# Performance work log

Measured on AMD Instinct MI355X. Metric: run time of the kernel, lower is better.

## Reference

```python
import jax, jax.numpy as jnp
import numpy as np

T, N, F, H = 64, 8192, 256, 256
LN_EPS = 1e-5


def setup_inputs() -> dict:
    key = jax.random.key(0)
    ks = jax.random.split(key, 8)
    bound = 1.0 / np.sqrt(H)  # torch RNNCell init: U(-1/sqrt(H), 1/sqrt(H))
    u = lambda k, shape: jax.random.uniform(k, shape, jnp.float32, -bound, bound)
    return {
        "X": jax.random.normal(ks[0], (T, N, F), jnp.float32),
        "W_ih": u(ks[1], (H, F)),
        "W_hh": u(ks[2], (H, H)),
        "b_ih": u(ks[3], (H,)),
        "b_hh": u(ks[4], (H,)),
        "ln_w": jnp.ones((H,), jnp.float32),
        "ln_b": jnp.zeros((H,), jnp.float32),
    }


def reference(X, W_ih, W_hh, b_ih, b_hh, ln_w, ln_b):
    # Precompute input projections for all steps: [T, N, H]
    Xw = jnp.einsum('tnf,hf->tnh', X, W_ih) + b_ih
    # init == 0 branch: h = X[0] @ W_ih^T + b_hh + b_ih  (no relu)
    h0 = Xw[0] + b_hh

    def step(h, xw_t):
        # RNNCell relu: relu(x W_ih^T + b_ih + h W_hh^T + b_hh)
        h_new = jax.nn.relu(xw_t + h @ W_hh.T + b_hh)
        return h_new, h_new

    _, outs = jax.lax.scan(step, h0, Xw)  # outs: [T, N, H]

    # LayerNorm over last dim
    mean = jnp.mean(outs, axis=-1, keepdims=True)
    var = jnp.var(outs, axis=-1, keepdims=True)
    outs = (outs - mean) * jax.lax.rsqrt(var + LN_EPS) * ln_w + ln_b
    # dropout: identity in eval mode
    return outs
```

## Files before the change

### kernel.cpp

```cpp
#include <hip/hip_runtime.h>
#include <hip/hip_bf16.h>

#define TSTEPS 64
#define NTOT   8192
#define FDIM   256
#define HDIM   256
#define ROWS   32
#define NTHR   256

typedef __attribute__((ext_vector_type(8))) short bf16x8;
typedef __attribute__((ext_vector_type(4))) float f32x4;

__device__ __forceinline__ short f2bf(float f) {
    union { float f; unsigned u; } v; v.f = f;
    unsigned r = v.u + 0x7FFFu + ((v.u >> 16) & 1u);
    return (short)(r >> 16);
}

__global__ __launch_bounds__(NTHR, 1)
void rnn_ln_fused(const float* __restrict__ X,
                  const float* __restrict__ W_ih,
                  const float* __restrict__ W_hh,
                  const float* __restrict__ b_ih,
                  const float* __restrict__ b_hh,
                  const float* __restrict__ ln_w,
                  const float* __restrict__ ln_b,
                  float* __restrict__ out)
{
    extern __shared__ char smem[];
    char*  xbuf = smem;
    char*  hbuf = smem + 16384;
    float* psum = (float*)(smem + 32768);
    float* mrs  = (float*)(smem + 32768 + 1024);

    const int tid = threadIdx.x;
    const int lane = tid & 63;
    const int wv  = tid >> 6;
    const int l15 = lane & 15;
    const int l4  = lane >> 4;
    const int n0  = blockIdx.x * ROWS;

    bf16x8 wih[8][4], whh[8][4];
    #pragma unroll
    for (int kk = 0; kk < 8; ++kk) {
        #pragma unroll
        for (int tc = 0; tc < 4; ++tc) {
            const int wr = wv*64 + tc*16 + l15;
            const int wk = kk*32 + l4*8;
            const float* p = W_ih + wr*FDIM + wk;
            const float* q = W_hh + wr*HDIM + wk;
            bf16x8 fi, fh;
            #pragma unroll
            for (int e = 0; e < 8; ++e) { fi[e] = f2bf(p[e]); fh[e] = f2bf(q[e]); }
            wih[kk][tc] = fi; whh[kk][tc] = fh;
        }
    }

    float bc[4], lw[4], lb[4];
    #pragma unroll
    for (int tc = 0; tc < 4; ++tc) {
        const int c = wv*64 + tc*16 + l15;
        bc[tc] = b_ih[c] + b_hh[c];
        lw[tc] = ln_w[c];
        lb[tc] = ln_b[c];
    }

    f32x4 acc[2][4];
    f32x4 xld[8];

    auto load_x = [&](int t) {
        const f32x4* base = (const f32x4*)(X + ((size_t)t * NTOT + n0) * FDIM);
        #pragma unroll
        for (int k = 0; k < 8; ++k) xld[k] = base[k*256 + tid];
    };
    auto store_x = [&]() {
        #pragma unroll
        for (int k = 0; k < 8; ++k) {
            const int row = 4*k + wv;
            int off = row*512 + (tid & 63)*8;
            off ^= (row & 7) << 4;
            unsigned lo = (unsigned)(unsigned short)f2bf(xld[k].x) |
                          ((unsigned)(unsigned short)f2bf(xld[k].y) << 16);
            unsigned hi = (unsigned)(unsigned short)f2bf(xld[k].z) |
                          ((unsigned)(unsigned short)f2bf(xld[k].w) << 16);
            uint2 v; v.x = lo; v.y = hi;
            *(uint2*)(xbuf + off) = v;
        }
    };
    auto mm = [&](const char* buf, const bf16x8 (&wf)[8][4]) {
        #pragma unroll
        for (int kk = 0; kk < 8; ++kk) {
            const int co = kk*64 + l4*16;
            const int r0 = l15, r1 = l15 + 16;
            const int sw = (l15 & 7) << 4;
            bf16x8 a0 = *(const bf16x8*)(buf + ((r0*512 + co) ^ sw));
            bf16x8 a1 = *(const bf16x8*)(buf + ((r1*512 + co) ^ sw));
            #pragma unroll
            for (int tc = 0; tc < 4; ++tc) {
                acc[0][tc] = __builtin_amdgcn_mfma_f32_16x16x32_bf16(a0, wf[kk][tc], acc[0][tc], 0, 0, 0);
                acc[1][tc] = __builtin_amdgcn_mfma_f32_16x16x32_bf16(a1, wf[kk][tc], acc[1][tc], 0, 0, 0);
            }
        }
    };
    auto zero_acc = [&]() {
        #pragma unroll
        for (int tr = 0; tr < 2; ++tr)
            #pragma unroll
            for (int tc = 0; tc < 4; ++tc) acc[tr][tc] = f32x4{0.f, 0.f, 0.f, 0.f};
    };

    load_x(0);
    store_x();
    __syncthreads();

    zero_acc();
    mm(xbuf, wih);
    load_x(1);
    __syncthreads();

    #pragma unroll
    for (int tr = 0; tr < 2; ++tr)
        #pragma unroll
        for (int j = 0; j < 4; ++j) {
            const int row = tr*16 + l4*4 + j;
            const int rs = row*512, sw = (row & 7) << 4;
            #pragma unroll
            for (int tc = 0; tc < 4; ++tc) {
                const int col = wv*64 + tc*16 + l15;
                *(short*)(hbuf + ((rs + col*2) ^ sw)) = f2bf(acc[tr][tc][j] + bc[tc]);
            }
        }
    store_x();
    __syncthreads();

    #pragma unroll 1
    for (int t = 0; t < TSTEPS; ++t) {
        if (t < 62) load_x(t + 2);

        mm(hbuf, whh);

        #pragma unroll
        for (int tr = 0; tr < 2; ++tr)
            #pragma unroll
            for (int tc = 0; tc < 4; ++tc) {
                f32x4 v = acc[tr][tc];
                #pragma unroll
                for (int j = 0; j < 4; ++j) v[j] = fmaxf(v[j] + bc[tc], 0.f);
                acc[tr][tc] = v;
            }

        float s[8], q[8];
        #pragma unroll
        for (int tr = 0; tr < 2; ++tr)
            #pragma unroll
            for (int j = 0; j < 4; ++j) {
                float a = 0.f, b = 0.f;
                #pragma unroll
                for (int tc = 0; tc < 4; ++tc) {
                    float v = acc[tr][tc][j];
                    a += v; b += v * v;
                }
                s[tr*4+j] = a; q[tr*4+j] = b;
            }
        #pragma unroll
        for (int m = 1; m < 16; m <<= 1) {
            #pragma unroll
            for (int i = 0; i < 8; ++i) {
                s[i] += __shfl_xor(s[i], m);
                q[i] += __shfl_xor(q[i], m);
            }
        }
        if (l15 == 0) {
            #pragma unroll
            for (int tr = 0; tr < 2; ++tr)
                #pragma unroll
                for (int j = 0; j < 4; ++j) {
                    const int row = tr*16 + l4*4 + j;
                    psum[(wv*32 + row)*2 + 0] = s[tr*4+j];
                    psum[(wv*32 + row)*2 + 1] = q[tr*4+j];
                }
        }
        __syncthreads();

        #pragma unroll
        for (int tr = 0; tr < 2; ++tr)
            #pragma unroll
            for (int j = 0; j < 4; ++j) {
                const int row = tr*16 + l4*4 + j;
                const int rs = row*512, sw = (row & 7) << 4;
                #pragma unroll
                for (int tc = 0; tc < 4; ++tc) {
                    const int col = wv*64 + tc*16 + l15;
                    *(short*)(hbuf + ((rs + col*2) ^ sw)) = f2bf(acc[tr][tc][j]);
                }
            }
        if (tid < 32) {
            float S = 0.f, Q = 0.f;
            #pragma unroll
            for (int k = 0; k < 4; ++k) {
                S += psum[(k*32 + tid)*2 + 0];
                Q += psum[(k*32 + tid)*2 + 1];
            }
            const float mean = S * (1.f/256.f);
            const float var  = Q * (1.f/256.f) - mean * mean;
            mrs[tid*2+0] = mean;
            mrs[tid*2+1] = rsqrtf(var + 1e-5f);
        }
        __syncthreads();

        float* op = out + ((size_t)t * NTOT + n0) * HDIM;
        #pragma unroll
        for (int tr = 0; tr < 2; ++tr)
            #pragma unroll
            for (int j = 0; j < 4; ++j) {
                const int row = tr*16 + l4*4 + j;
                const float mean = mrs[row*2+0];
                const float rstd = mrs[row*2+1];
                #pragma unroll
                for (int tc = 0; tc < 4; ++tc) {
                    const int col = wv*64 + tc*16 + l15;
                    op[row*HDIM + col] = (acc[tr][tc][j] - mean) * rstd * lw[tc] + lb[tc];
                }
            }

        if (t < 63) {
            zero_acc();
            mm(xbuf, wih);
            if (t < 62) {
                __syncthreads();
                store_x();
            }
        }
    }
}

extern "C" void kernel_launch(void* const* d_in, const int* in_sizes, int n_in,
                              void* d_out, int out_size, void* d_ws, size_t ws_size,
                              hipStream_t stream) {
    const float* X   = (const float*)d_in[0];
    const float* Wih = (const float*)d_in[1];
    const float* Whh = (const float*)d_in[2];
    const float* bih = (const float*)d_in[3];
    const float* bhh = (const float*)d_in[4];
    const float* lnw = (const float*)d_in[5];
    const float* lnb = (const float*)d_in[6];
    float* out = (float*)d_out;

    const size_t shmem = 2*16384 + 1024 + 256;
    rnn_ln_fused<<<dim3(NTOT / ROWS), dim3(NTHR), shmem, stream>>>(
        X, Wih, Whh, bih, bhh, lnw, lnb, out);
}
```

Baseline: 340.0 us.

## Use 8 waves per block with double-buffered x/h LDS and lighter barriers

```diff
diff --git a/kernel.cpp b/kernel.cpp
--- a/kernel.cpp
+++ b/kernel.cpp
@@ -6,7 +6,7 @@
 #define FDIM   256
 #define HDIM   256
 #define ROWS   32
-#define NTHR   256
+#define NTHR   512
 
 typedef __attribute__((ext_vector_type(8))) short bf16x8;
 typedef __attribute__((ext_vector_type(4))) float f32x4;
@@ -17,7 +17,12 @@
     return (short)(r >> 16);
 }
 
-__global__ __launch_bounds__(NTHR, 1)
+__device__ __forceinline__ void bar_lgkm() {
+    asm volatile("s_waitcnt lgkmcnt(0)" ::: "memory");
+    __builtin_amdgcn_s_barrier();
+}
+
+__global__ __launch_bounds__(NTHR, 2)
 void rnn_ln_fused(const float* __restrict__ X,
                   const float* __restrict__ W_ih,
                   const float* __restrict__ W_hh,
@@ -27,25 +32,27 @@
                   const float* __restrict__ ln_b,
                   float* __restrict__ out)
 {
-    extern __shared__ char smem[];
-    char*  xbuf = smem;
-    char*  hbuf = smem + 16384;
-    float* psum = (float*)(smem + 32768);
-    float* mrs  = (float*)(smem + 32768 + 1024);
-
-    const int tid = threadIdx.x;
+    __shared__ char smem[4*16384 + 2048 + 256];
+    char* xb0 = smem;
+    char* xb1 = smem + 16384;
+    char* hb0 = smem + 32768;
+    char* hb1 = smem + 49152;
+    float* psum = (float*)(smem + 65536);
+    float* mrs  = (float*)(smem + 65536 + 2048);
+
+    const int tid  = threadIdx.x;
     const int lane = tid & 63;
-    const int wv  = tid >> 6;
-    const int l15 = lane & 15;
-    const int l4  = lane >> 4;
-    const int n0  = blockIdx.x * ROWS;
-
-    bf16x8 wih[8][4], whh[8][4];
+    const int wv   = tid >> 6;
+    const int l15  = lane & 15;
+    const int l4   = lane >> 4;
+    const int n0   = blockIdx.x * ROWS;
+
+    bf16x8 wih[8][2], whh[8][2];
     #pragma unroll
     for (int kk = 0; kk < 8; ++kk) {
         #pragma unroll
-        for (int tc = 0; tc < 4; ++tc) {
-            const int wr = wv*64 + tc*16 + l15;
+        for (int tc = 0; tc < 2; ++tc) {
+            const int wr = wv*32 + tc*16 + l15;
             const int wk = kk*32 + l4*8;
             const float* p = W_ih + wr*FDIM + wk;
             const float* q = W_hh + wr*HDIM + wk;
@@ -56,28 +63,28 @@
         }
     }
 
-    float bc[4], lw[4], lb[4];
+    float bc[2], lw[2], lb[2];
     #pragma unroll
-    for (int tc = 0; tc < 4; ++tc) {
-        const int c = wv*64 + tc*16 + l15;
+    for (int tc = 0; tc < 2; ++tc) {
+        const int c = wv*32 + tc*16 + l15;
         bc[tc] = b_ih[c] + b_hh[c];
         lw[tc] = ln_w[c];
         lb[tc] = ln_b[c];
     }
 
-    f32x4 acc[2][4];
-    f32x4 xld[8];
+    f32x4 acc[2][2];
+    f32x4 xld[4];
 
     auto load_x = [&](int t) {
         const f32x4* base = (const f32x4*)(X + ((size_t)t * NTOT + n0) * FDIM);
         #pragma unroll
-        for (int k = 0; k < 8; ++k) xld[k] = base[k*256 + tid];
-    };
-    auto store_x = [&]() {
-        #pragma unroll
-        for (int k = 0; k < 8; ++k) {
-            const int row = 4*k + wv;
-            int off = row*512 + (tid & 63)*8;
+        for (int k = 0; k < 4; ++k) xld[k] = base[k*512 + tid];
+    };
+    auto store_x = [&](char* xbuf) {
+        #pragma unroll
+        for (int k = 0; k < 4; ++k) {
+            const int row = 8*k + wv;
+            int off = row*512 + lane*8;
             off ^= (row & 7) << 4;
             unsigned lo = (unsigned)(unsigned short)f2bf(xld[k].x) |
                           ((unsigned)(unsigned short)f2bf(xld[k].y) << 16);
@@ -87,7 +94,7 @@
             *(uint2*)(xbuf + off) = v;
         }
     };
-    auto mm = [&](const char* buf, const bf16x8 (&wf)[8][4]) {
+    auto mm = [&](const char* buf, const bf16x8 (&wf)[8][2]) {
         #pragma unroll
         for (int kk = 0; kk < 8; ++kk) {
             const int co = kk*64 + l4*16;
@@ -96,7 +103,7 @@
             bf16x8 a0 = *(const bf16x8*)(buf + ((r0*512 + co) ^ sw));
             bf16x8 a1 = *(const bf16x8*)(buf + ((r1*512 + co) ^ sw));
             #pragma unroll
-            for (int tc = 0; tc < 4; ++tc) {
+            for (int tc = 0; tc < 2; ++tc) {
                 acc[0][tc] = __builtin_amdgcn_mfma_f32_16x16x32_bf16(a0, wf[kk][tc], acc[0][tc], 0, 0, 0);
                 acc[1][tc] = __builtin_amdgcn_mfma_f32_16x16x32_bf16(a1, wf[kk][tc], acc[1][tc], 0, 0, 0);
             }
@@ -106,82 +113,9 @@
         #pragma unroll
         for (int tr = 0; tr < 2; ++tr)
             #pragma unroll
-            for (int tc = 0; tc < 4; ++tc) acc[tr][tc] = f32x4{0.f, 0.f, 0.f, 0.f};
-    };
-
-    load_x(0);
-    store_x();
-    __syncthreads();
-
-    zero_acc();
-    mm(xbuf, wih);
-    load_x(1);
-    __syncthreads();
-
-    #pragma unroll
-    for (int tr = 0; tr < 2; ++tr)
-        #pragma unroll
-        for (int j = 0; j < 4; ++j) {
-            const int row = tr*16 + l4*4 + j;
-            const int rs = row*512, sw = (row & 7) << 4;
-            #pragma unroll
-            for (int tc = 0; tc < 4; ++tc) {
-                const int col = wv*64 + tc*16 + l15;
-                *(short*)(hbuf + ((rs + col*2) ^ sw)) = f2bf(acc[tr][tc][j] + bc[tc]);
-            }
-        }
-    store_x();
-    __syncthreads();
-
-    #pragma unroll 1
-    for (int t = 0; t < TSTEPS; ++t) {
-        if (t < 62) load_x(t + 2);
-
-        mm(hbuf, whh);
-
-        #pragma unroll
-        for (int tr = 0; tr < 2; ++tr)
-            #pragma unroll
-            for (int tc = 0; tc < 4; ++tc) {
-                f32x4 v = acc[tr][tc];
-                #pragma unroll
-                for (int j = 0; j < 4; ++j) v[j] = fmaxf(v[j] + bc[tc], 0.f);
-                acc[tr][tc] = v;
-            }
-
-        float s[8], q[8];
-        #pragma unroll
-        for (int tr = 0; tr < 2; ++tr)
-            #pragma unroll
-            for (int j = 0; j < 4; ++j) {
-                float a = 0.f, b = 0.f;
-                #pragma unroll
-                for (int tc = 0; tc < 4; ++tc) {
-                    float v = acc[tr][tc][j];
-                    a += v; b += v * v;
-                }
-                s[tr*4+j] = a; q[tr*4+j] = b;
-            }
-        #pragma unroll
-        for (int m = 1; m < 16; m <<= 1) {
-            #pragma unroll
-            for (int i = 0; i < 8; ++i) {
-                s[i] += __shfl_xor(s[i], m);
-                q[i] += __shfl_xor(q[i], m);
-            }
-        }
-        if (l15 == 0) {
-            #pragma unroll
-            for (int tr = 0; tr < 2; ++tr)
-                #pragma unroll
-                for (int j = 0; j < 4; ++j) {
-                    const int row = tr*16 + l4*4 + j;
-                    psum[(wv*32 + row)*2 + 0] = s[tr*4+j];
-                    psum[(wv*32 + row)*2 + 1] = q[tr*4+j];
-                }
-        }
-        __syncthreads();
-
+            for (int tc = 0; tc < 2; ++tc) acc[tr][tc] = f32x4{0.f, 0.f, 0.f, 0.f};
+    };
+    auto write_h = [&](char* hbuf, bool addbias) {
         #pragma unroll
         for (int tr = 0; tr < 2; ++tr)
             #pragma unroll
@@ -189,24 +123,99 @@
                 const int row = tr*16 + l4*4 + j;
                 const int rs = row*512, sw = (row & 7) << 4;
                 #pragma unroll
-                for (int tc = 0; tc < 4; ++tc) {
-                    const int col = wv*64 + tc*16 + l15;
-                    *(short*)(hbuf + ((rs + col*2) ^ sw)) = f2bf(acc[tr][tc][j]);
-                }
-            }
-        if (tid < 32) {
-            float S = 0.f, Q = 0.f;
-            #pragma unroll
-            for (int k = 0; k < 4; ++k) {
-                S += psum[(k*32 + tid)*2 + 0];
-                Q += psum[(k*32 + tid)*2 + 1];
-            }
-            const float mean = S * (1.f/256.f);
-            const float var  = Q * (1.f/256.f) - mean * mean;
-            mrs[tid*2+0] = mean;
-            mrs[tid*2+1] = rsqrtf(var + 1e-5f);
-        }
-        __syncthreads();
+                for (int tc = 0; tc < 2; ++tc) {
+                    const int col = wv*32 + tc*16 + l15;
+                    float v = acc[tr][tc][j];
+                    if (addbias) v += bc[tc];
+                    *(short*)(hbuf + ((rs + col*2) ^ sw)) = f2bf(v);
+                }
+            }
+    };
+
+    load_x(0);
+    store_x(xb0);
+    load_x(1);
+    bar_lgkm();
+
+    zero_acc();
+    mm(xb0, wih);
+    store_x(xb1);
+    load_x(2);
+    write_h(hb0, true);
+    bar_lgkm();
+
+    #pragma unroll 1
+    for (int t = 0; t < TSTEPS; ++t) {
+        char* hcur = (t & 1) ? hb1 : hb0;
+        char* hnxt = (t & 1) ? hb0 : hb1;
+        char* xrd  = (t & 1) ? xb0 : xb1;
+        char* xwr  = (t & 1) ? xb1 : xb0;
+
+        mm(hcur, whh);
+
+        #pragma unroll
+        for (int tr = 0; tr < 2; ++tr)
+            #pragma unroll
+            for (int tc = 0; tc < 2; ++tc) {
+                f32x4 v = acc[tr][tc];
+                #pragma unroll
+                for (int j = 0; j < 4; ++j) v[j] = fmaxf(v[j] + bc[tc], 0.f);
+                acc[tr][tc] = v;
+            }
+
+        {
+            float s[8], q[8];
+            #pragma unroll
+            for (int tr = 0; tr < 2; ++tr)
+                #pragma unroll
+                for (int j = 0; j < 4; ++j) {
+                    float a = acc[tr][0][j] + acc[tr][1][j];
+                    float b = acc[tr][0][j]*acc[tr][0][j] + acc[tr][1][j]*acc[tr][1][j];
+                    s[tr*4+j] = a; q[tr*4+j] = b;
+                }
+            #pragma unroll
+            for (int m = 1; m < 16; m <<= 1) {
+                #pragma unroll
+                for (int i = 0; i < 8; ++i) {
+                    s[i] += __shfl_xor(s[i], m);
+                    q[i] += __shfl_xor(q[i], m);
+                }
+            }
+            if (l15 == 0) {
+                #pragma unroll
+                for (int tr = 0; tr < 2; ++tr)
+                    #pragma unroll
+                    for (int j = 0; j < 4; ++j) {
+                        const int row = tr*16 + l4*4 + j;
+                        float2 w; w.x = s[tr*4+j]; w.y = q[tr*4+j];
+                        *(float2*)(psum + (row*8 + wv)*2) = w;
+                    }
+            }
+        }
+
+        write_h(hnxt, false);
+
+        bar_lgkm();
+
+        if (tid < 256) {
+            const int row = tid >> 3, p = tid & 7;
+            const float2 v = *(const float2*)(psum + (row*8 + p)*2);
+            float S = v.x, Q = v.y;
+            S += __shfl_xor(S, 1); Q += __shfl_xor(Q, 1);
+            S += __shfl_xor(S, 2); Q += __shfl_xor(Q, 2);
+            S += __shfl_xor(S, 4); Q += __shfl_xor(Q, 4);
+            if (p == 0) {
+                const float mean = S * (1.f/256.f);
+                const float var  = Q * (1.f/256.f) - mean * mean;
+                float2 w; w.x = mean; w.y = rsqrtf(var + 1e-5f);
+                *(float2*)(mrs + row*2) = w;
+            }
+        }
+        if (t < 62) store_x(xwr);
+
+        bar_lgkm();
+
+        if (t < 61) load_x(t + 3);
 
         float* op = out + ((size_t)t * NTOT + n0) * HDIM;
         #pragma unroll
@@ -214,22 +223,17 @@
             #pragma unroll
             for (int j = 0; j < 4; ++j) {
                 const int row = tr*16 + l4*4 + j;
-                const float mean = mrs[row*2+0];
-                const float rstd = mrs[row*2+1];
-                #pragma unroll
-                for (int tc = 0; tc < 4; ++tc) {
-                    const int col = wv*64 + tc*16 + l15;
-                    op[row*HDIM + col] = (acc[tr][tc][j] - mean) * rstd * lw[tc] + lb[tc];
+                const float2 ms = *(const float2*)(mrs + row*2);
+                #pragma unroll
+                for (int tc = 0; tc < 2; ++tc) {
+                    const int col = wv*32 + tc*16 + l15;
+                    op[row*HDIM + col] = (acc[tr][tc][j] - ms.x) * ms.y * lw[tc] + lb[tc];
                 }
             }
 
         if (t < 63) {
             zero_acc();
-            mm(xbuf, wih);
-            if (t < 62) {
-                __syncthreads();
-                store_x();
-            }
+            mm(xrd, wih);
         }
     }
 }
@@ -246,7 +250,6 @@
     const float* lnb = (const float*)d_in[6];
     float* out = (float*)d_out;
 
-    const size_t shmem = 2*16384 + 1024 + 256;
-    rnn_ln_fused<<<dim3(NTOT / ROWS), dim3(NTHR), shmem, stream>>>(
+    rnn_ln_fused<<<dim3(NTOT / ROWS), dim3(NTHR), 0, stream>>>(
         X, Wih, Whh, bih, bhh, lnw, lnb, out);
 }
```

After: 493.4 us. 45.1% more time.
